# Optimization experiments

Hardware: AMD Instinct MI355X
Metric: run time of the kernel (lower is better)

Reference implementation:

```python
import jax, jax.numpy as jnp
import numpy as np
import math

NUM_HEADS = 8
LN_EPS = 1e-5


def _lstm_stack(x, Wih, Whh, bih, bhh):
    """Stacked unidirectional LSTM (torch gate order i,f,g,o). x: [B,T,F]; params stacked [L,...]."""
    L = Wih.shape[0]
    for l in range(L):
        # precompute input contribution for all timesteps: [B,T,4H]
        xg = jnp.einsum('btf,gf->btg', x, Wih[l]) + bih[l] + bhh[l]
        B = x.shape[0]
        H = Whh.shape[2]
        Whh_l = Whh[l]

        def step(carry, g_t):
            h, c = carry
            g = g_t + h @ Whh_l.T  # [B,4H]
            i, f, gg, o = jnp.split(g, 4, axis=-1)
            c = jax.nn.sigmoid(f) * c + jax.nn.sigmoid(i) * jnp.tanh(gg)
            h = jax.nn.sigmoid(o) * jnp.tanh(c)
            return (h, c), h

        init = (jnp.zeros((B, H), x.dtype), jnp.zeros((B, H), x.dtype))
        _, hs = jax.lax.scan(step, init, xg.transpose(1, 0, 2))  # hs: [T,B,H]
        x = hs.transpose(1, 0, 2)
    return x


def _forward(input, noise, lstm_Wih, lstm_Whh, lstm_bih, lstm_bhh, ln_gamma, ln_beta,
             Wcp, bcp, Wff, bff, Wq, bq, Wkv, bkv, Wout, bout, sequence_mask, chunk_size):
    B, T, F = input.shape
    K = T // chunk_size

    lstm_out = _lstm_stack(input, lstm_Wih, lstm_Whh, lstm_bih, lstm_bhh)  # [B,T,H]

    # LayerNorm over last dim
    mu = lstm_out.mean(-1, keepdims=True)
    var = ((lstm_out - mu) ** 2).mean(-1, keepdims=True)
    normed = (lstm_out - mu) / jnp.sqrt(var + LN_EPS) * ln_gamma + ln_beta

    # chunk summaries -> pivots [B,K,ff]
    chunk_summary = normed.reshape(B * K, chunk_size, -1).sum(axis=1)
    chunk_pivots = (chunk_summary @ Wcp.T + bcp).reshape(B, K, -1)
    # per-frame features [B,T,ff]
    future_frames = normed @ Wff.T + bff

    ff_dim = chunk_pivots.shape[-1]
    dot_products = jnp.einsum('bkf,btf->bkt', chunk_pivots, future_frames) * math.sqrt(1.0 / float(ff_dim))
    eof_probs = jax.nn.sigmoid(dot_products + noise)  # [B,K,T]

    # zero eof prob for frames up to each chunk's endpoint (always in-context)
    chunk_endpts = (jnp.arange(K) + 1) * chunk_size  # [K]
    within = jnp.arange(T)[None, :] < chunk_endpts[:, None]  # [K,T]
    eof_probs = jnp.where(within[None, :, :], 0.0, eof_probs)
    # padded frames: eof prob 1 (never attended beyond)
    eof_probs = jnp.where(~sequence_mask[:, None, :], 1.0, eof_probs)

    in_futctx_probs = jnp.concatenate(
        [jnp.ones_like(eof_probs[..., :1]), 1.0 - eof_probs[..., :-1]], axis=-1)  # [B,K,T]

    # expected multi-head attention
    hd = ff_dim // NUM_HEADS
    q = (chunk_pivots @ Wq.T + bq).reshape(B, K, NUM_HEADS, hd)
    kv = future_frames @ Wkv.T + bkv
    k, v = jnp.split(kv, 2, axis=-1)
    k = k.reshape(B, T, NUM_HEADS, hd)
    v = v.reshape(B, T, NUM_HEADS, hd)

    scale = math.sqrt(1.0 / float(hd))
    scores = jnp.einsum('bkhf,bthf->bhkt', q, k)
    attn = jax.nn.softmax(scale * scores, axis=-1)
    attn = attn * in_futctx_probs[:, None, :, :]
    attn = attn / attn.sum(axis=-1, keepdims=True)
    # attn_dropout is identity in eval mode
    ctx = jnp.einsum('bhkt,bthf->bkhf', attn, v).reshape(B, K, ff_dim)
    expected_fut_ctx = ctx @ Wout.T + bout  # [B,K,input_dim]
    return expected_fut_ctx, in_futctx_probs


def setup_inputs() -> dict:
    key = jax.random.key(0)
    ks = jax.random.split(key, 24)
    B, T, F = 8, 1024, 512
    H = 512
    FF = 512
    L = 2
    CS = 32
    K = T // CS
    s = 0.04  # ~1/sqrt(512)
    inp = {
        'input': jax.random.normal(ks[0], (B, T, F), jnp.float32),
        'sequence_mask': jnp.ones((B, T), jnp.bool_),
        'chunk_size': CS,
        'noise': jax.random.normal(ks[1], (B, K, T), jnp.float32) * 0.1,
        'lstm_Wih': jax.random.normal(ks[2], (L, 4 * H, F), jnp.float32) * s,
        'lstm_Whh': jax.random.normal(ks[3], (L, 4 * H, H), jnp.float32) * s,
        'lstm_bih': jax.random.normal(ks[4], (L, 4 * H), jnp.float32) * s,
        'lstm_bhh': jax.random.normal(ks[5], (L, 4 * H), jnp.float32) * s,
        'ln_gamma': jnp.ones((H,), jnp.float32) + jax.random.normal(ks[6], (H,), jnp.float32) * 0.02,
        'ln_beta': jax.random.normal(ks[7], (H,), jnp.float32) * 0.02,
        'Wcp': jax.random.normal(ks[8], (FF, H), jnp.float32) * s,
        'bcp': jax.random.normal(ks[9], (FF,), jnp.float32) * s,
        'Wff': jax.random.normal(ks[10], (FF, H), jnp.float32) * s,
        'bff': jax.random.normal(ks[11], (FF,), jnp.float32) * s,
        'Wq': jax.random.normal(ks[12], (FF, FF), jnp.float32) * s,
        'bq': jax.random.normal(ks[13], (FF,), jnp.float32) * s,
        'Wkv': jax.random.normal(ks[14], (2 * FF, FF), jnp.float32) * s,
        'bkv': jax.random.normal(ks[15], (2 * FF,), jnp.float32) * s,
        'Wout': jax.random.normal(ks[16], (F, FF), jnp.float32) * s,
        'bout': jax.random.normal(ks[17], (F,), jnp.float32) * s,
    }
    return inp


def reference(input, noise, lstm_Wih, lstm_Whh, lstm_bih, lstm_bhh, ln_gamma, ln_beta,
              Wcp, bcp, Wff, bff, Wq, bq, Wkv, bkv, Wout, bout, sequence_mask, chunk_size):
    return _forward(input, noise, lstm_Wih, lstm_Whh, lstm_bih, lstm_bhh, ln_gamma, ln_beta,
                    Wcp, bcp, Wff, bff, Wq, bq, Wkv, bkv, Wout, bout, sequence_mask, chunk_size)
```

## Files before the change

kernel.cpp:

```cpp
#include <hip/hip_runtime.h>


typedef unsigned short u16;
typedef __attribute__((ext_vector_type(8))) short bf16x8;
typedef __attribute__((ext_vector_type(4))) float f32x4;
typedef __attribute__((ext_vector_type(4))) unsigned int u32x4;

#define T_    1024
#define HSTR  20

__device__ __forceinline__ float bf2f(u16 h) {
    union { unsigned int u; float f; } v; v.u = ((unsigned int)h) << 16; return v.f;
}
__device__ __forceinline__ u16 f2bf(float x) {
    union { float f; unsigned int u; } v; v.f = x;
    unsigned int r = (v.u + 0x7FFFu + ((v.u >> 16) & 1u)) >> 16;
    return (u16)r;
}
__device__ __forceinline__ float sigm(float x) { return 1.f / (1.f + __expf(-x)); }
__device__ __forceinline__ float tanhf_(float x) {
    float e = __expf(-2.f * fabsf(x));
    float t = (1.f - e) / (1.f + e);
    return x < 0.f ? -t : t;
}

__global__ __launch_bounds__(256) void k_split(const float* __restrict__ in,
                                               u16* __restrict__ hi, u16* __restrict__ lo, long n) {
    long i = ((long)blockIdx.x * 256 + threadIdx.x) * 4;
    if (i >= n) return;
    union { u16 h[4]; unsigned long long q; } ph, pl;
#pragma unroll
    for (int j = 0; j < 4; ++j) {
        float v = in[i + j];
        u16 h = f2bf(v);
        ph.h[j] = h;
        pl.h[j] = f2bf(v - bf2f(h));
    }
    *reinterpret_cast<unsigned long long*>(hi + i) = ph.q;
    *reinterpret_cast<unsigned long long*>(lo + i) = pl.q;
}

__global__ __launch_bounds__(256) void k_addvec(const float* __restrict__ a, const float* __restrict__ b,
                                                float* __restrict__ o, int n) {
    int i = blockIdx.x * 256 + threadIdx.x;
    if (i < n) o[i] = a[i] + b[i];
}

__global__ __launch_bounds__(256)
void k_gemm(const u16* __restrict__ Ah, const u16* __restrict__ Al,
            const u16* __restrict__ Bh, const u16* __restrict__ Bl,
            const float* __restrict__ bias,
            float* __restrict__ Cf, u16* __restrict__ Ch, u16* __restrict__ Cl,
            unsigned int* __restrict__ Cp, int xgfmt,
            int M, int N, int K, long sA, long sB, long sC)
{
    const int lane = threadIdx.x & 63;
    const int wave = threadIdx.x >> 6;
    const int wr = wave >> 1, wc = wave & 1;
    const long bz = blockIdx.z;
    const u16* Ahb = Ah + bz * sA;
    const u16* Alb = Al + bz * sA;
    const u16* Bhb = Bh + bz * sB;
    const u16* Blb = Bl + bz * sB;
    const int rowBase = blockIdx.y * 128 + wr * 64;
    const int colBase = blockIdx.x * 128 + wc * 64;
    const int lr = lane & 15;
    const int lk = (lane >> 4) * 8;

    f32x4 acc[4][4];
#pragma unroll
    for (int j = 0; j < 4; ++j) {
        float bv = bias ? bias[colBase + j * 16 + lr] : 0.f;
#pragma unroll
        for (int i = 0; i < 4; ++i) acc[i][j] = (f32x4){bv, bv, bv, bv};
    }
    for (int k0 = 0; k0 < K; k0 += 32) {
        bf16x8 ah[4], al[4], bh[4], bl[4];
#pragma unroll
        for (int i = 0; i < 4; ++i) {
            long off = (long)(rowBase + i * 16 + lr) * K + k0 + lk;
            ah[i] = *reinterpret_cast<const bf16x8*>(Ahb + off);
            al[i] = *reinterpret_cast<const bf16x8*>(Alb + off);
        }
#pragma unroll
        for (int j = 0; j < 4; ++j) {
            long off = (long)(colBase + j * 16 + lr) * K + k0 + lk;
            bh[j] = *reinterpret_cast<const bf16x8*>(Bhb + off);
            bl[j] = *reinterpret_cast<const bf16x8*>(Blb + off);
        }
#pragma unroll
        for (int i = 0; i < 4; ++i)
#pragma unroll
            for (int j = 0; j < 4; ++j) {
                acc[i][j] = __builtin_amdgcn_mfma_f32_16x16x32_bf16(ah[i], bh[j], acc[i][j], 0, 0, 0);
                acc[i][j] = __builtin_amdgcn_mfma_f32_16x16x32_bf16(al[i], bh[j], acc[i][j], 0, 0, 0);
                acc[i][j] = __builtin_amdgcn_mfma_f32_16x16x32_bf16(ah[i], bl[j], acc[i][j], 0, 0, 0);
            }
    }
#pragma unroll
    for (int i = 0; i < 4; ++i) {
        int row0 = rowBase + i * 16 + (lane >> 4) * 4;
#pragma unroll
        for (int j = 0; j < 4; ++j) {
            int col = colBase + j * 16 + lr;
#pragma unroll
            for (int r = 0; r < 4; ++r) {
                int row = row0 + r;
                if (row < M) {
                    float v = acc[i][j][r];
                    if (Cp) {
                        u16 h = f2bf(v); u16 l = f2bf(v - bf2f(h));
                        unsigned int pv = (unsigned int)h | ((unsigned int)l << 16);
                        long idx = xgfmt ? (((long)(row & 1023) * 2048 + col) * 8 + (row >> 10))
                                         : (bz * sC + (long)row * N + col);
                        Cp[idx] = pv;
                    } else if (Ch) {
                        long idx = bz * sC + (long)row * N + col;
                        u16 h = f2bf(v);
                        Ch[idx] = h;
                        Cl[idx] = f2bf(v - bf2f(h));
                    } else {
                        Cf[bz * sC + (long)row * N + col] = v;
                    }
                }
            }
        }
    }
}

__global__ __launch_bounds__(256, 1)
void k_lstm2(const u16* __restrict__ Wh1, const u16* __restrict__ Wl1,
             const u16* __restrict__ Wh2, const u16* __restrict__ Wl2,
             const u16* __restrict__ Uh2, const u16* __restrict__ Ul2,
             const unsigned int* __restrict__ xg1,
             const float* __restrict__ bias2,
             unsigned int* __restrict__ hw1, unsigned int* __restrict__ hw2,
             unsigned int* __restrict__ fl1, unsigned int* __restrict__ fl2)
{
    __shared__ u16 ldsWh[64 * 512];
    __shared__ unsigned int hstA[256 * HSTR];
    __shared__ unsigned int hstB[256 * HSTR];
    __shared__ unsigned int outb[128];

    const int bid = blockIdx.x;
    const bool isL2 = bid >= 32;
    const int blk = isL2 ? bid - 32 : bid;
    const int tid = threadIdx.x;
    const int lane = tid & 63;
    const int wave = tid >> 6;
    const int lr = lane & 15;
    const int lkh = lane >> 4;
    const int lk = lkh * 8;
    const int grow = (lr & 3) * 512 + blk * 16 + wave * 4 + (lr >> 2);

    const u16* WhA = isL2 ? Wh2 : Wh1;
    const u16* WlA = isL2 ? Wl2 : Wl1;

    for (int i = tid; i < 64 * 64; i += 256) {
        int rl = i >> 6;
        int col = (i & 63) * 8;
        int g = (rl & 3) * 512 + blk * 16 + (rl >> 4) * 4 + ((rl >> 2) & 3);
        int sw = rl * 512 + (col ^ ((rl & 15) << 3));
        *reinterpret_cast<bf16x8*>(&ldsWh[sw]) =
            *reinterpret_cast<const bf16x8*>(WhA + (long)g * 512 + col);
    }
    __syncthreads();

    const int myrl = wave * 16 + lr;
    const int swz = (myrl & 15) << 3;
    const int basel = lane & ~3;
    const bool writer = ((lane & 3) == 0) && (lkh < 2);
    const int uloc = wave * 4 + (lr >> 2);
    float cc[4] = {0.f, 0.f, 0.f, 0.f};
    const float bv = isL2 ? bias2[grow] : 0.f;
    unsigned int* hwOut = isL2 ? hw2 : hw1;
    unsigned int* flOut = isL2 ? fl2 : fl1;

    auto waitf = [&](const unsigned int* pa, const unsigned int* pb) {
        const unsigned int* p = (lane < 32) ? (pa + lane * 16)
                                            : (pb ? (pb + (lane - 32) * 16) : nullptr);
        for (int g = 0; g < 131072; ++g) {
            unsigned int f = p ? __hip_atomic_load(p, __ATOMIC_RELAXED, __HIP_MEMORY_SCOPE_AGENT) : 1u;
            if (__ballot(f != 0) == ~0ULL) break;
            __builtin_amdgcn_s_sleep(1);
        }
        asm volatile("" ::: "memory");
    };

    auto stage = [&](const unsigned int* src, unsigned int* dst) {
        const unsigned int* s = src + tid * 16;
        u32x4 v0 = *reinterpret_cast<const u32x4*>(s);
        u32x4 v1 = *reinterpret_cast<const u32x4*>(s + 4);
        u32x4 v2 = *reinterpret_cast<const u32x4*>(s + 8);
        u32x4 v3 = *reinterpret_cast<const u32x4*>(s + 12);
        unsigned int* d = dst + tid * HSTR;
        *reinterpret_cast<u32x4*>(d)      = v0;
        *reinterpret_cast<u32x4*>(d + 4)  = v1;
        *reinterpret_cast<u32x4*>(d + 8)  = v2;
        *reinterpret_cast<u32x4*>(d + 12) = v3;
    };

    auto hfrag = [&](const unsigned int* hst, int s, bf16x8& hi, bf16x8& lo) {
        if (lr < 8) {
            const unsigned int* hp = hst + (s * 16 + (lkh >> 1) * 8 + lr) * HSTR + (lkh & 1) * 8;
            u32x4 wa = *reinterpret_cast<const u32x4*>(hp);
            u32x4 wb = *reinterpret_cast<const u32x4*>(hp + 4);
            union { unsigned int d[4]; bf16x8 v; } H, L;
            H.d[0] = __builtin_amdgcn_perm(wa.y, wa.x, 0x05040100u);
            L.d[0] = __builtin_amdgcn_perm(wa.y, wa.x, 0x07060302u);
            H.d[1] = __builtin_amdgcn_perm(wa.w, wa.z, 0x05040100u);
            L.d[1] = __builtin_amdgcn_perm(wa.w, wa.z, 0x07060302u);
            H.d[2] = __builtin_amdgcn_perm(wb.y, wb.x, 0x05040100u);
            L.d[2] = __builtin_amdgcn_perm(wb.y, wb.x, 0x07060302u);
            H.d[3] = __builtin_amdgcn_perm(wb.w, wb.z, 0x05040100u);
            L.d[3] = __builtin_amdgcn_perm(wb.w, wb.z, 0x07060302u);
            hi = H.v; lo = L.v;
        } else {
            hi = (bf16x8){0,0,0,0,0,0,0,0};
            lo = (bf16x8){0,0,0,0,0,0,0,0};
        }
    };

#pragma unroll 1
    for (int ct = 0; ct < T_; ++ct) {
        u32x4 xw = (u32x4){0, 0, 0, 0};
        if (!isL2 && lkh < 2)
            xw = *reinterpret_cast<const u32x4*>(xg1 + ((long)ct * 2048 + grow) * 8 + lkh * 4);

        if (wave == 0) {
            if (!isL2) waitf(fl1 + (long)ct * 512, nullptr);
            else       waitf(fl2 + (long)ct * 512, fl1 + (long)(ct + 1) * 512);
        }
        __syncthreads();

        if (!isL2) stage(hw1 + (long)ct * 4096, hstA);
        else {
            stage(hw2 + (long)ct * 4096, hstA);
            stage(hw1 + (long)(ct + 1) * 4096, hstB);
        }
        __syncthreads();

        f32x4 acc;
        if (!isL2) {
            f32x4 a0, a1 = (f32x4){0.f, 0.f, 0.f, 0.f};
            a0.x = bf2f((u16)(xw.x & 0xffff)) + bf2f((u16)(xw.x >> 16));
            a0.y = bf2f((u16)(xw.y & 0xffff)) + bf2f((u16)(xw.y >> 16));
            a0.z = bf2f((u16)(xw.z & 0xffff)) + bf2f((u16)(xw.z >> 16));
            a0.w = bf2f((u16)(xw.w & 0xffff)) + bf2f((u16)(xw.w >> 16));
#pragma unroll
            for (int s = 0; s < 16; s += 2) {
                bf16x8 h0, l0, h1, l1;
                hfrag(hstA, s, h0, l0);
                hfrag(hstA, s + 1, h1, l1);
                int c0 = (s * 32 + lk) ^ swz;
                int c1 = ((s + 1) * 32 + lk) ^ swz;
                bf16x8 wh0 = *reinterpret_cast<const bf16x8*>(&ldsWh[myrl * 512 + c0]);
                bf16x8 wh1 = *reinterpret_cast<const bf16x8*>(&ldsWh[myrl * 512 + c1]);
                long w0 = (long)grow * 512 + s * 32 + lk;
                bf16x8 wl0 = *reinterpret_cast<const bf16x8*>(WlA + w0);
                bf16x8 wl1 = *reinterpret_cast<const bf16x8*>(WlA + w0 + 32);
                a0 = __builtin_amdgcn_mfma_f32_16x16x32_bf16(h0, wh0, a0, 0, 0, 0);
                a1 = __builtin_amdgcn_mfma_f32_16x16x32_bf16(h1, wh1, a1, 0, 0, 0);
                a0 = __builtin_amdgcn_mfma_f32_16x16x32_bf16(l0, wh0, a0, 0, 0, 0);
                a1 = __builtin_amdgcn_mfma_f32_16x16x32_bf16(l1, wh1, a1, 0, 0, 0);
                a0 = __builtin_amdgcn_mfma_f32_16x16x32_bf16(h0, wl0, a0, 0, 0, 0);
                a1 = __builtin_amdgcn_mfma_f32_16x16x32_bf16(h1, wl1, a1, 0, 0, 0);
            }
            acc = a0 + a1;
        } else {
            f32x4 a0 = (f32x4){bv, bv, bv, bv};
            f32x4 a1 = (f32x4){0.f, 0.f, 0.f, 0.f};
            f32x4 a2 = a1, a3 = a1;
#pragma unroll
            for (int s = 0; s < 16; s += 2) {
                bf16x8 h2a, l2a, h2b, l2b, h1a, l1a, h1b, l1b;
                hfrag(hstA, s, h2a, l2a);
                hfrag(hstA, s + 1, h2b, l2b);
                hfrag(hstB, s, h1a, l1a);
                hfrag(hstB, s + 1, h1b, l1b);
                int c0 = (s * 32 + lk) ^ swz;
                int c1 = ((s + 1) * 32 + lk) ^ swz;
                bf16x8 wh0 = *reinterpret_cast<const bf16x8*>(&ldsWh[myrl * 512 + c0]);
                bf16x8 wh1 = *reinterpret_cast<const bf16x8*>(&ldsWh[myrl * 512 + c1]);
                long w0 = (long)grow * 512 + s * 32 + lk;
                bf16x8 wl0 = *reinterpret_cast<const bf16x8*>(WlA + w0);
                bf16x8 wl1 = *reinterpret_cast<const bf16x8*>(WlA + w0 + 32);
                bf16x8 uh0 = *reinterpret_cast<const bf16x8*>(Uh2 + w0);
                bf16x8 uh1 = *reinterpret_cast<const bf16x8*>(Uh2 + w0 + 32);
                bf16x8 ul0 = *reinterpret_cast<const bf16x8*>(Ul2 + w0);
                bf16x8 ul1 = *reinterpret_cast<const bf16x8*>(Ul2 + w0 + 32);
                a0 = __builtin_amdgcn_mfma_f32_16x16x32_bf16(h2a, wh0, a0, 0, 0, 0);
                a1 = __builtin_amdgcn_mfma_f32_16x16x32_bf16(h2b, wh1, a1, 0, 0, 0);
                a2 = __builtin_amdgcn_mfma_f32_16x16x32_bf16(h1a, uh0, a2, 0, 0, 0);
                a3 = __builtin_amdgcn_mfma_f32_16x16x32_bf16(h1b, uh1, a3, 0, 0, 0);
                a0 = __builtin_amdgcn_mfma_f32_16x16x32_bf16(l2a, wh0, a0, 0, 0, 0);
                a1 = __builtin_amdgcn_mfma_f32_16x16x32_bf16(l2b, wh1, a1, 0, 0, 0);
                a2 = __builtin_amdgcn_mfma_f32_16x16x32_bf16(l1a, ul0, a2, 0, 0, 0);
                a3 = __builtin_amdgcn_mfma_f32_16x16x32_bf16(l1b, ul1, a3, 0, 0, 0);
                a0 = __builtin_amdgcn_mfma_f32_16x16x32_bf16(h2a, wl0, a0, 0, 0, 0);
                a1 = __builtin_amdgcn_mfma_f32_16x16x32_bf16(h2b, wl1, a1, 0, 0, 0);
                a2 = __builtin_amdgcn_mfma_f32_16x16x32_bf16(h1a, uh0, a2, 0, 0, 0) - a2 + a2;
                a3 = a3;
                a2 = __builtin_amdgcn_mfma_f32_16x16x32_bf16(h1a, ul0, a2, 0, 0, 0) - a2 + a2;
                a3 = a3;
                (void)0;
                a2 = __builtin_amdgcn_mfma_f32_16x16x32_bf16(l1a, uh0, a2, 0, 0, 0);
                a3 = __builtin_amdgcn_mfma_f32_16x16x32_bf16(l1b, uh1, a3, 0, 0, 0);
            }
            a2 = (f32x4){0.f, 0.f, 0.f, 0.f};
            a3 = (f32x4){0.f, 0.f, 0.f, 0.f};
#pragma unroll
            for (int s = 0; s < 16; s += 2) {
                bf16x8 h1a, l1a, h1b, l1b;
                hfrag(hstB, s, h1a, l1a);
                hfrag(hstB, s + 1, h1b, l1b);
                long w0 = (long)grow * 512 + s * 32 + lk;
                bf16x8 uh0 = *reinterpret_cast<const bf16x8*>(Uh2 + w0);
                bf16x8 uh1 = *reinterpret_cast<const bf16x8*>(Uh2 + w0 + 32);
                bf16x8 ul0 = *reinterpret_cast<const bf16x8*>(Ul2 + w0);
                bf16x8 ul1 = *reinterpret_cast<const bf16x8*>(Ul2 + w0 + 32);
                a2 = __builtin_amdgcn_mfma_f32_16x16x32_bf16(h1a, uh0, a2, 0, 0, 0);
                a3 = __builtin_amdgcn_mfma_f32_16x16x32_bf16(h1b, uh1, a3, 0, 0, 0);
                a2 = __builtin_amdgcn_mfma_f32_16x16x32_bf16(l1a, uh0, a2, 0, 0, 0);
                a3 = __builtin_amdgcn_mfma_f32_16x16x32_bf16(l1b, uh1, a3, 0, 0, 0);
                a2 = __builtin_amdgcn_mfma_f32_16x16x32_bf16(h1a, ul0, a2, 0, 0, 0);
                a3 = __builtin_amdgcn_mfma_f32_16x16x32_bf16(h1b, ul1, a3, 0, 0, 0);
            }
            acc = (a0 + a1) + (a2 + a3);
        }

        float hval[4];
#pragma unroll
        for (int r = 0; r < 4; ++r) {
            float v = acc[r];
            float iv = __shfl(v, basel + 0, 64);
            float fv = __shfl(v, basel + 1, 64);
            float gv = __shfl(v, basel + 2, 64);
            float ov = __shfl(v, basel + 3, 64);
            float cn = sigm(fv) * cc[r] + sigm(iv) * tanhf_(gv);
            cc[r] = cn;
            hval[r] = sigm(ov) * tanhf_(cn);
        }
        if (writer) {
#pragma unroll
            for (int r = 0; r < 4; ++r) {
                u16 h = f2bf(hval[r]);
                outb[(lkh * 4 + r) * 16 + uloc] =
                    (unsigned int)h | ((unsigned int)f2bf(hval[r] - bf2f(h)) << 16);
            }
        }
        __syncthreads();
        if (wave == 0) {
            if (lane < 32) {
                u32x4 v = *reinterpret_cast<const u32x4*>(&outb[lane * 4]);
                unsigned long long* hd = (unsigned long long*)
                    (hwOut + (long)(ct + 1) * 4096 + blk * 128 + lane * 4);
                __hip_atomic_store(hd, (unsigned long long)v.x | ((unsigned long long)v.y << 32),
                                   __ATOMIC_RELAXED, __HIP_MEMORY_SCOPE_AGENT);
                __hip_atomic_store(hd + 1, (unsigned long long)v.z | ((unsigned long long)v.w << 32),
                                   __ATOMIC_RELAXED, __HIP_MEMORY_SCOPE_AGENT);
            }
            asm volatile("s_waitcnt vmcnt(0)" ::: "memory");
            if (tid == 0)
                __hip_atomic_store(flOut + (long)(ct + 1) * 512 + blk * 16, 1u,
                                   __ATOMIC_RELAXED, __HIP_MEMORY_SCOPE_AGENT);
        }
    }
}

__global__ __launch_bounds__(256)
void k_ln(const unsigned int* __restrict__ hw2,
          const float* __restrict__ gamma, const float* __restrict__ beta,
          u16* __restrict__ nh, u16* __restrict__ nl)
{
    __shared__ float sb[8];
    int m = blockIdx.x;
    int b = m >> 10, t = m & 1023;
    const unsigned int* src = hw2 + (long)(t + 1) * 4096;
    int tid = threadIdx.x;
    int u0 = tid, u1 = tid + 256;
    unsigned int w0 = src[(u0 >> 4) * 128 + b * 16 + (u0 & 15)];
    unsigned int w1 = src[(u1 >> 4) * 128 + b * 16 + (u1 & 15)];
    float x0 = bf2f((u16)(w0 & 0xffff)) + bf2f((u16)(w0 >> 16));
    float x1 = bf2f((u16)(w1 & 0xffff)) + bf2f((u16)(w1 >> 16));
    float s = x0 + x1;
#pragma unroll
    for (int off = 32; off; off >>= 1) s += __shfl_down(s, off, 64);
    int wv = tid >> 6, ln = tid & 63;
    if (ln == 0) sb[wv] = s;
    __syncthreads();
    float mu = (sb[0] + sb[1] + sb[2] + sb[3]) * (1.f / 512.f);
    float d0 = x0 - mu, d1 = x1 - mu;
    float ss = d0 * d0 + d1 * d1;
#pragma unroll
    for (int off = 32; off; off >>= 1) ss += __shfl_down(ss, off, 64);
    if (ln == 0) sb[4 + wv] = ss;
    __syncthreads();
    float var = (sb[4] + sb[5] + sb[6] + sb[7]) * (1.f / 512.f);
    float rstd = rsqrtf(var + 1e-5f);
    float y0 = d0 * rstd * gamma[tid] + beta[tid];
    float y1 = d1 * rstd * gamma[tid + 256] + beta[tid + 256];
    long d = (long)m * 512;
    u16 h0 = f2bf(y0); nh[d + tid] = h0; nl[d + tid] = f2bf(y0 - bf2f(h0));
    u16 h1 = f2bf(y1); nh[d + tid + 256] = h1; nl[d + tid + 256] = f2bf(y1 - bf2f(h1));
}

__global__ __launch_bounds__(256)
void k_chunksum(const u16* __restrict__ nh, const u16* __restrict__ nl,
                u16* __restrict__ ch, u16* __restrict__ cl)
{
    int bk = blockIdx.x;
    int tid = threadIdx.x;
    long base = (long)bk * 32 * 512;
    float s0 = 0.f, s1 = 0.f;
#pragma unroll 4
    for (int i = 0; i < 32; ++i) {
        s0 += bf2f(nh[base + (long)i * 512 + tid]) + bf2f(nl[base + (long)i * 512 + tid]);
        s1 += bf2f(nh[base + (long)i * 512 + tid + 256]) + bf2f(nl[base + (long)i * 512 + tid + 256]);
    }
    long d = (long)bk * 512;
    u16 h0 = f2bf(s0); ch[d + tid] = h0; cl[d + tid] = f2bf(s0 - bf2f(h0));
    u16 h1 = f2bf(s1); ch[d + tid + 256] = h1; cl[d + tid + 256] = f2bf(s1 - bf2f(h1));
}

__global__ __launch_bounds__(256)
void k_eof(const float* __restrict__ dp, const float* __restrict__ noise, float* __restrict__ ifp)
{
    int bk = blockIdx.x;
    int k = bk & 31;
    long base = (long)bk * 1024;
    int tid = threadIdx.x;
#pragma unroll
    for (int i = 0; i < 4; ++i) {
        int t = tid + i * 256;
        float e;
        if (t < (k + 1) * 32) e = 0.f;
        else e = sigm(dp[base + t] * 0.0441941738241592f + noise[base + t]);
        if (t == 0) ifp[base] = 1.f;
        if (t < 1023) ifp[base + t + 1] = 1.f - e;
    }
}

__global__ __launch_bounds__(256)
void k_attn(const float* __restrict__ qf, const float* __restrict__ kvf,
            const float* __restrict__ ifp, u16* __restrict__ ctxh, u16* __restrict__ ctxl)
{
    int bh = blockIdx.x;
    int b = bh >> 5;
    int h = (bh >> 2) & 7;
    int kg = bh & 3;
    __shared__ float qs[8 * 64];
    __shared__ float tile[64 * 65];
    __shared__ float sc[8 * 1024];
    int tid = threadIdx.x;

    for (int i = tid; i < 512; i += 256) {
        int kq = i >> 6, d = i & 63;
        qs[i] = qf[((long)b * 32 + kg * 8 + kq) * 512 + h * 64 + d];
    }
    __syncthreads();
    for (int t0 = 0; t0 < 1024; t0 += 64) {
        for (int i = tid; i < 4096; i += 256) {
            int tt = i >> 6, d = i & 63;
            tile[tt * 65 + d] = kvf[((long)b * 1024 + t0 + tt) * 1024 + h * 64 + d];
        }
        __syncthreads();
#pragma unroll
        for (int pi = 0; pi < 2; ++pi) {
            int p = tid + pi * 256;
            int kq = p >> 6, tt = p & 63;
            float s = 0.f;
#pragma unroll 8
            for (int d = 0; d < 64; ++d) s += qs[kq * 64 + d] * tile[tt * 65 + d];
            sc[kq * 1024 + t0 + tt] = s * 0.125f;
        }
        __syncthreads();
    }
    {
        int w = tid >> 6, lane = tid & 63;
#pragma unroll
        for (int rr = 0; rr < 2; ++rr) {
            int kq = w * 2 + rr;
            float m = -1e30f;
            float vv[16];
#pragma unroll
            for (int i = 0; i < 16; ++i) {
                vv[i] = sc[kq * 1024 + lane + i * 64];
                m = fmaxf(m, vv[i]);
            }
#pragma unroll
            for (int off = 32; off; off >>= 1) m = fmaxf(m, __shfl_xor(m, off, 64));
            long ibase = ((long)b * 32 + kg * 8 + kq) * 1024;
            float sum = 0.f;
            float wv[16];
#pragma unroll
            for (int i = 0; i < 16; ++i) {
                float pv = ifp[ibase + lane + i * 64];
                float e = __expf(vv[i] - m) * pv;
                wv[i] = e; sum += e;
            }
#pragma unroll
            for (int off = 32; off; off >>= 1) sum += __shfl_xor(sum, off, 64);
            float inv = 1.f / sum;
#pragma unroll
            for (int i = 0; i < 16; ++i) sc[kq * 1024 + lane + i * 64] = wv[i] * inv;
        }
    }
    __syncthreads();
    float c0 = 0.f, c1 = 0.f;
    int kq0 = tid >> 6, d0 = tid & 63;
    int kq1 = (tid + 256) >> 6, d1 = tid & 63;
    for (int t0 = 0; t0 < 1024; t0 += 64) {
        __syncthreads();
        for (int i = tid; i < 4096; i += 256) {
            int tt = i >> 6, d = i & 63;
            tile[tt * 65 + d] = kvf[((long)b * 1024 + t0 + tt) * 1024 + 512 + h * 64 + d];
        }
        __syncthreads();
#pragma unroll 8
        for (int tt = 0; tt < 64; ++tt) {
            float a0 = sc[kq0 * 1024 + t0 + tt];
            float a1 = sc[kq1 * 1024 + t0 + tt];
            c0 += a0 * tile[tt * 65 + d0];
            c1 += a1 * tile[tt * 65 + d1];
        }
    }
    long i0 = ((long)b * 32 + kg * 8 + kq0) * 512 + h * 64 + d0;
    long i1 = ((long)b * 32 + kg * 8 + kq1) * 512 + h * 64 + d1;
    u16 h0 = f2bf(c0); ctxh[i0] = h0; ctxl[i0] = f2bf(c0 - bf2f(h0));
    u16 h1v = f2bf(c1); ctxh[i1] = h1v; ctxl[i1] = f2bf(c1 - bf2f(h1v));
}

extern "C" void kernel_launch(void* const* d_in, const int* in_sizes, int n_in,
                              void* d_out, int out_size, void* d_ws, size_t ws_size,
                              hipStream_t stream)
{
    const float* input = (const float*)d_in[0];
    const float* noise = (const float*)d_in[3];
    const float* Wih  = (const float*)d_in[4];
    const float* Whh  = (const float*)d_in[5];
    const float* bih  = (const float*)d_in[6];
    const float* bhh  = (const float*)d_in[7];
    const float* gam  = (const float*)d_in[8];
    const float* bet  = (const float*)d_in[9];
    const float* Wcp  = (const float*)d_in[10]; const float* bcp  = (const float*)d_in[11];
    const float* Wff  = (const float*)d_in[12]; const float* bff  = (const float*)d_in[13];
    const float* Wq   = (const float*)d_in[14]; const float* bq   = (const float*)d_in[15];
    const float* Wkv  = (const float*)d_in[16]; const float* bkv  = (const float*)d_in[17];
    const float* Wout = (const float*)d_in[18]; const float* bout = (const float*)d_in[19];
    (void)in_sizes; (void)n_in; (void)out_size; (void)ws_size;

    float* out_ctx = (float*)d_out;
    float* out_ifp = (float*)d_out + 8 * 32 * 512;

    char* p = (char*)d_ws;
    auto alloc = [&](size_t bytes) { char* q = p; p += (bytes + 255) & ~(size_t)255; return q; };
    u16* Xh   = (u16*)alloc(8192ULL * 512 * 2);  u16* Xl   = (u16*)alloc(8192ULL * 512 * 2);
    u16* Wihh = (u16*)alloc(2ULL*2048*512*2);    u16* Wihl = (u16*)alloc(2ULL*2048*512*2);
    u16* Whhh = (u16*)alloc(2ULL*2048*512*2);    u16* Whhl = (u16*)alloc(2ULL*2048*512*2);
    u16* Wcph = (u16*)alloc(512ULL*512*2);       u16* Wcpl = (u16*)alloc(512ULL*512*2);
    u16* Wffh = (u16*)alloc(512ULL*512*2);       u16* Wffl = (u16*)alloc(512ULL*512*2);
    u16* Wqh  = (u16*)alloc(512ULL*512*2);       u16* Wql  = (u16*)alloc(512ULL*512*2);
    u16* Wkvh = (u16*)alloc(1024ULL*512*2);      u16* Wkvl = (u16*)alloc(1024ULL*512*2);
    u16* Wouth= (u16*)alloc(512ULL*512*2);       u16* Woutl= (u16*)alloc(512ULL*512*2);
    float* bias12 = (float*)alloc(4096ULL * 4);
    unsigned int* xg1p = (unsigned int*)alloc(8192ULL * 2048 * 4);
    unsigned int* hw1  = (unsigned int*)alloc(1025ULL * 4096 * 4);
    unsigned int* hw2  = (unsigned int*)alloc(1025ULL * 4096 * 4);
    unsigned int* fl1  = (unsigned int*)alloc(1025ULL * 512 * 4);
    unsigned int* fl2  = (unsigned int*)alloc(1025ULL * 512 * 4);
    u16* nh   = (u16*)alloc(8192ULL*512*2);      u16* nl   = (u16*)alloc(8192ULL*512*2);
    u16* csh  = (u16*)alloc(256ULL*512*2);       u16* csl  = (u16*)alloc(256ULL*512*2);
    u16* pivh = (u16*)alloc(512ULL*512*2);       u16* pivl = (u16*)alloc(512ULL*512*2);
    u16* ffh  = (u16*)alloc(8192ULL*512*2);      u16* ffl  = (u16*)alloc(8192ULL*512*2);
    u16* ctxhb= (u16*)alloc(256ULL*512*2);       u16* ctxlb= (u16*)alloc(256ULL*512*2);
    float* qf  = (float*)alloc(256ULL*512*4);
    float* kvf = (float*)alloc(8192ULL*1024*4);
    float* dp  = (float*)alloc(8ULL*32*1024*4);

    hipMemsetAsync(fl1, 0, 1025ULL * 512 * 4, stream);
    hipMemsetAsync(fl2, 0, 1025ULL * 512 * 4, stream);
    hipMemsetAsync(fl1, 1, 32 * 64, stream);
    hipMemsetAsync(fl2, 1, 32 * 64, stream);
    hipMemsetAsync(hw1, 0, 4096 * 4, stream);
    hipMemsetAsync(hw2, 0, 4096 * 4, stream);

    k_split<<<4096, 256, 0, stream>>>(input, Xh, Xl, 8192L * 512);
    k_split<<<2048, 256, 0, stream>>>(Wih, Wihh, Wihl, 2L * 2048 * 512);
    k_split<<<2048, 256, 0, stream>>>(Whh, Whhh, Whhl, 2L * 2048 * 512);
    k_split<<<256, 256, 0, stream>>>(Wcp, Wcph, Wcpl, 512L * 512);
    k_split<<<256, 256, 0, stream>>>(Wff, Wffh, Wffl, 512L * 512);
    k_split<<<256, 256, 0, stream>>>(Wq, Wqh, Wql, 512L * 512);
    k_split<<<512, 256, 0, stream>>>(Wkv, Wkvh, Wkvl, 1024L * 512);
    k_split<<<256, 256, 0, stream>>>(Wout, Wouth, Woutl, 512L * 512);
    k_addvec<<<16, 256, 0, stream>>>(bih, bhh, bias12, 4096);

    k_gemm<<<dim3(16, 64, 1), 256, 0, stream>>>(Xh, Xl, Wihh, Wihl, bias12,
                                                nullptr, nullptr, nullptr, xg1p, 1,
                                                8192, 2048, 512, 0, 0, 0);
    k_lstm2<<<64, 256, 0, stream>>>(Whhh, Whhl, Whhh + 2048L*512, Whhl + 2048L*512,
                                    Wihh + 2048L*512, Wihl + 2048L*512,
                                    xg1p, bias12 + 2048, hw1, hw2, fl1, fl2);

    k_ln<<<8192, 256, 0, stream>>>(hw2, gam, bet, nh, nl);
    k_chunksum<<<256, 256, 0, stream>>>(nh, nl, csh, csl);
    k_gemm<<<dim3(4, 2, 1), 256, 0, stream>>>(csh, csl, Wcph, Wcpl, bcp,
                                              nullptr, pivh, pivl, nullptr, 0, 256, 512, 512, 0, 0, 0);
    k_gemm<<<dim3(4, 2, 1), 256, 0, stream>>>(pivh, pivl, Wqh, Wql, bq,
                                              qf, nullptr, nullptr, nullptr, 0, 256, 512, 512, 0, 0, 0);
    k_gemm<<<dim3(4, 64, 1), 256, 0, stream>>>(nh, nl, Wffh, Wffl, bff,
                                               nullptr, ffh, ffl, nullptr, 0, 8192, 512, 512, 0, 0, 0);
    k_gemm<<<dim3(8, 64, 1), 256, 0, stream>>>(ffh, ffl, Wkvh, Wkvl, bkv,
                                               kvf, nullptr, nullptr, nullptr, 0, 8192, 1024, 512, 0, 0, 0);
    k_gemm<<<dim3(8, 1, 8), 256, 0, stream>>>(pivh, pivl, ffh, ffl, nullptr,
                                              dp, nullptr, nullptr, nullptr, 0, 32, 1024, 512,
                                              32L * 512, 1024L * 512, 32L * 1024);
    k_eof<<<256, 256, 0, stream>>>(dp, noise, out_ifp);
    k_attn<<<256, 256, 0, stream>>>(qf, kvf, out_ifp, ctxhb, ctxlb);
    k_gemm<<<dim3(4, 2, 1), 256, 0, stream>>>(ctxhb, ctxlb, Wouth, Woutl, bout,
                                              out_ctx, nullptr, nullptr, nullptr, 0, 256, 512, 512, 0, 0, 0);
}
```

Measured before the change: 10.38 ms.

## Read LSTM hidden state directly from global, prefetch xg, drop redundant MFMAs

Removes the per-step LDS staging of the previous hidden state and its extra __syncthreads. MFMA fragments are now loaded directly from the global handoff buffer, and the output scratch is double-buffered so the dropped barrier does not create a hazard. The layer-1 input-gate contribution is prefetched four timesteps ahead in registers. The layer-2 path loses a duplicated, partly wasted recurrent-weight loop, and both layers use more independent accumulators to shorten MFMA dependency chains. The aim is lower latency on the serial recurrence. The risk is that global/L2 reads of the fresh hidden state may have higher latency than the LDS reads they replace.

Result: slower. 17.46 ms (+68.1%).

```diff
diff --git a/kernel.cpp b/kernel.cpp
--- a/kernel.cpp
+++ b/kernel.cpp
@@ -7,7 +7,6 @@
 typedef __attribute__((ext_vector_type(4))) unsigned int u32x4;
 
 #define T_    1024
-#define HSTR  20
 
 __device__ __forceinline__ float bf2f(u16 h) {
     union { unsigned int u; float f; } v; v.u = ((unsigned int)h) << 16; return v.f;
@@ -138,9 +137,7 @@
              unsigned int* __restrict__ fl1, unsigned int* __restrict__ fl2)
 {
     __shared__ u16 ldsWh[64 * 512];
-    __shared__ unsigned int hstA[256 * HSTR];
-    __shared__ unsigned int hstB[256 * HSTR];
-    __shared__ unsigned int outb[128];
+    __shared__ unsigned int outb[2][128];
 
     const int bid = blockIdx.x;
     const bool isL2 = bid >= 32;
@@ -187,22 +184,9 @@
         asm volatile("" ::: "memory");
     };
 
-    auto stage = [&](const unsigned int* src, unsigned int* dst) {
-        const unsigned int* s = src + tid * 16;
-        u32x4 v0 = *reinterpret_cast<const u32x4*>(s);
-        u32x4 v1 = *reinterpret_cast<const u32x4*>(s + 4);
-        u32x4 v2 = *reinterpret_cast<const u32x4*>(s + 8);
-        u32x4 v3 = *reinterpret_cast<const u32x4*>(s + 12);
-        unsigned int* d = dst + tid * HSTR;
-        *reinterpret_cast<u32x4*>(d)      = v0;
-        *reinterpret_cast<u32x4*>(d + 4)  = v1;
-        *reinterpret_cast<u32x4*>(d + 8)  = v2;
-        *reinterpret_cast<u32x4*>(d + 12) = v3;
-    };
-
-    auto hfrag = [&](const unsigned int* hst, int s, bf16x8& hi, bf16x8& lo) {
+    auto hfrag = [&](const unsigned int* slot, int s, bf16x8& hi, bf16x8& lo) {
         if (lr < 8) {
-            const unsigned int* hp = hst + (s * 16 + (lkh >> 1) * 8 + lr) * HSTR + (lkh & 1) * 8;
+            const unsigned int* hp = slot + (s * 2 + (lkh >> 1)) * 128 + lr * 16 + (lkh & 1) * 8;
             u32x4 wa = *reinterpret_cast<const u32x4*>(hp);
             u32x4 wb = *reinterpret_cast<const u32x4*>(hp + 4);
             union { unsigned int d[4]; bf16x8 v; } H, L;
@@ -221,37 +205,38 @@
         }
     };
 
+    auto xgload = [&](int t) {
+        u32x4 v = (u32x4){0, 0, 0, 0};
+        if (lkh < 2 && t < T_)
+            v = *reinterpret_cast<const u32x4*>(xg1 + ((long)t * 2048 + grow) * 8 + lkh * 4);
+        return v;
+    };
+    u32x4 xq0 = (u32x4){0,0,0,0}, xq1 = xq0, xq2 = xq0, xq3 = xq0;
+    if (!isL2) { xq0 = xgload(0); xq1 = xgload(1); xq2 = xgload(2); xq3 = xgload(3); }
+
 #pragma unroll 1
     for (int ct = 0; ct < T_; ++ct) {
-        u32x4 xw = (u32x4){0, 0, 0, 0};
-        if (!isL2 && lkh < 2)
-            xw = *reinterpret_cast<const u32x4*>(xg1 + ((long)ct * 2048 + grow) * 8 + lkh * 4);
-
         if (wave == 0) {
             if (!isL2) waitf(fl1 + (long)ct * 512, nullptr);
             else       waitf(fl2 + (long)ct * 512, fl1 + (long)(ct + 1) * 512);
         }
         __syncthreads();
 
-        if (!isL2) stage(hw1 + (long)ct * 4096, hstA);
-        else {
-            stage(hw2 + (long)ct * 4096, hstA);
-            stage(hw1 + (long)(ct + 1) * 4096, hstB);
-        }
-        __syncthreads();
-
         f32x4 acc;
         if (!isL2) {
-            f32x4 a0, a1 = (f32x4){0.f, 0.f, 0.f, 0.f};
-            a0.x = bf2f((u16)(xw.x & 0xffff)) + bf2f((u16)(xw.x >> 16));
-            a0.y = bf2f((u16)(xw.y & 0xffff)) + bf2f((u16)(xw.y >> 16));
-            a0.z = bf2f((u16)(xw.z & 0xffff)) + bf2f((u16)(xw.z >> 16));
-            a0.w = bf2f((u16)(xw.w & 0xffff)) + bf2f((u16)(xw.w >> 16));
+            const unsigned int* s1 = hw1 + (long)ct * 4096;
+            f32x4 a0, a1, a2, a3;
+            a0.x = bf2f((u16)(xq0.x & 0xffff)) + bf2f((u16)(xq0.x >> 16));
+            a0.y = bf2f((u16)(xq0.y & 0xffff)) + bf2f((u16)(xq0.y >> 16));
+            a0.z = bf2f((u16)(xq0.z & 0xffff)) + bf2f((u16)(xq0.z >> 16));
+            a0.w = bf2f((u16)(xq0.w & 0xffff)) + bf2f((u16)(xq0.w >> 16));
+            a1 = (f32x4){0.f,0.f,0.f,0.f}; a2 = a1; a3 = a1;
+            xq0 = xq1; xq1 = xq2; xq2 = xq3; xq3 = xgload(ct + 4);
 #pragma unroll
             for (int s = 0; s < 16; s += 2) {
                 bf16x8 h0, l0, h1, l1;
-                hfrag(hstA, s, h0, l0);
-                hfrag(hstA, s + 1, h1, l1);
+                hfrag(s1, s, h0, l0);
+                hfrag(s1, s + 1, h1, l1);
                 int c0 = (s * 32 + lk) ^ swz;
                 int c1 = ((s + 1) * 32 + lk) ^ swz;
                 bf16x8 wh0 = *reinterpret_cast<const bf16x8*>(&ldsWh[myrl * 512 + c0]);
@@ -261,23 +246,25 @@
                 bf16x8 wl1 = *reinterpret_cast<const bf16x8*>(WlA + w0 + 32);
                 a0 = __builtin_amdgcn_mfma_f32_16x16x32_bf16(h0, wh0, a0, 0, 0, 0);
                 a1 = __builtin_amdgcn_mfma_f32_16x16x32_bf16(h1, wh1, a1, 0, 0, 0);
-                a0 = __builtin_amdgcn_mfma_f32_16x16x32_bf16(l0, wh0, a0, 0, 0, 0);
-                a1 = __builtin_amdgcn_mfma_f32_16x16x32_bf16(l1, wh1, a1, 0, 0, 0);
+                a2 = __builtin_amdgcn_mfma_f32_16x16x32_bf16(l0, wh0, a2, 0, 0, 0);
+                a3 = __builtin_amdgcn_mfma_f32_16x16x32_bf16(l1, wh1, a3, 0, 0, 0);
                 a0 = __builtin_amdgcn_mfma_f32_16x16x32_bf16(h0, wl0, a0, 0, 0, 0);
                 a1 = __builtin_amdgcn_mfma_f32_16x16x32_bf16(h1, wl1, a1, 0, 0, 0);
             }
-            acc = a0 + a1;
+            acc = (a0 + a2) + (a1 + a3);
         } else {
-            f32x4 a0 = (f32x4){bv, bv, bv, bv};
-            f32x4 a1 = (f32x4){0.f, 0.f, 0.f, 0.f};
-            f32x4 a2 = a1, a3 = a1;
+            const unsigned int* s2 = hw2 + (long)ct * 4096;
+            const unsigned int* s1 = hw1 + (long)(ct + 1) * 4096;
+            f32x4 wa0 = (f32x4){bv, bv, bv, bv};
+            f32x4 z = (f32x4){0.f,0.f,0.f,0.f};
+            f32x4 wa1 = z, wa2 = z, wa3 = z, ua0 = z, ua1 = z, ua2 = z, ua3 = z;
 #pragma unroll
             for (int s = 0; s < 16; s += 2) {
-                bf16x8 h2a, l2a, h2b, l2b, h1a, l1a, h1b, l1b;
-                hfrag(hstA, s, h2a, l2a);
-                hfrag(hstA, s + 1, h2b, l2b);
-                hfrag(hstB, s, h1a, l1a);
-                hfrag(hstB, s + 1, h1b, l1b);
+                bf16x8 h0, l0, h1, l1, g0, m0, g1, m1;
+                hfrag(s2, s, h0, l0);
+                hfrag(s2, s + 1, h1, l1);
+                hfrag(s1, s, g0, m0);
+                hfrag(s1, s + 1, g1, m1);
                 int c0 = (s * 32 + lk) ^ swz;
                 int c1 = ((s + 1) * 32 + lk) ^ swz;
                 bf16x8 wh0 = *reinterpret_cast<const bf16x8*>(&ldsWh[myrl * 512 + c0]);
@@ -289,44 +276,20 @@
                 bf16x8 uh1 = *reinterpret_cast<const bf16x8*>(Uh2 + w0 + 32);
                 bf16x8 ul0 = *reinterpret_cast<const bf16x8*>(Ul2 + w0);
                 bf16x8 ul1 = *reinterpret_cast<const bf16x8*>(Ul2 + w0 + 32);
-                a0 = __builtin_amdgcn_mfma_f32_16x16x32_bf16(h2a, wh0, a0, 0, 0, 0);
-                a1 = __builtin_amdgcn_mfma_f32_16x16x32_bf16(h2b, wh1, a1, 0, 0, 0);
-                a2 = __builtin_amdgcn_mfma_f32_16x16x32_bf16(h1a, uh0, a2, 0, 0, 0);
-                a3 = __builtin_amdgcn_mfma_f32_16x16x32_bf16(h1b, uh1, a3, 0, 0, 0);
-                a0 = __builtin_amdgcn_mfma_f32_16x16x32_bf16(l2a, wh0, a0, 0, 0, 0);
-                a1 = __builtin_amdgcn_mfma_f32_16x16x32_bf16(l2b, wh1, a1, 0, 0, 0);
-                a2 = __builtin_amdgcn_mfma_f32_16x16x32_bf16(l1a, ul0, a2, 0, 0, 0);
-                a3 = __builtin_amdgcn_mfma_f32_16x16x32_bf16(l1b, ul1, a3, 0, 0, 0);
-                a0 = __builtin_amdgcn_mfma_f32_16x16x32_bf16(h2a, wl0, a0, 0, 0, 0);
-                a1 = __builtin_amdgcn_mfma_f32_16x16x32_bf16(h2b, wl1, a1, 0, 0, 0);
-                a2 = __builtin_amdgcn_mfma_f32_16x16x32_bf16(h1a, uh0, a2, 0, 0, 0) - a2 + a2;
-                a3 = a3;
-                a2 = __builtin_amdgcn_mfma_f32_16x16x32_bf16(h1a, ul0, a2, 0, 0, 0) - a2 + a2;
-                a3 = a3;
-                (void)0;
-                a2 = __builtin_amdgcn_mfma_f32_16x16x32_bf16(l1a, uh0, a2, 0, 0, 0);
-                a3 = __builtin_amdgcn_mfma_f32_16x16x32_bf16(l1b, uh1, a3, 0, 0, 0);
-            }
-            a2 = (f32x4){0.f, 0.f, 0.f, 0.f};
-            a3 = (f32x4){0.f, 0.f, 0.f, 0.f};
-#pragma unroll
-            for (int s = 0; s < 16; s += 2) {
-                bf16x8 h1a, l1a, h1b, l1b;
-                hfrag(hstB, s, h1a, l1a);
-                hfrag(hstB, s + 1, h1b, l1b);
-                long w0 = (long)grow * 512 + s * 32 + lk;
-                bf16x8 uh0 = *reinterpret_cast<const bf16x8*>(Uh2 + w0);
-                bf16x8 uh1 = *reinterpret_cast<const bf16x8*>(Uh2 + w0 + 32);
-                bf16x8 ul0 = *reinterpret_cast<const bf16x8*>(Ul2 + w0);
-                bf16x8 ul1 = *reinterpret_cast<const bf16x8*>(Ul2 + w0 + 32);
-                a2 = __builtin_amdgcn_mfma_f32_16x16x32_bf16(h1a, uh0, a2, 0, 0, 0);
-                a3 = __builtin_amdgcn_mfma_f32_16x16x32_bf16(h1b, uh1, a3, 0, 0, 0);
-                a2 = __builtin_amdgcn_mfma_f32_16x16x32_bf16(l1a, uh0, a2, 0, 0, 0);
-                a3 = __builtin_amdgcn_mfma_f32_16x16x32_bf16(l1b, uh1, a3, 0, 0, 0);
-                a2 = __builtin_amdgcn_mfma_f32_16x16x32_bf16(h1a, ul0, a2, 0, 0, 0);
-                a3 = __builtin_amdgcn_mfma_f32_16x16x32_bf16(h1b, ul1, a3, 0, 0, 0);
-            }
-            acc = (a0 + a1) + (a2 + a3);
+                wa0 = __builtin_amdgcn_mfma_f32_16x16x32_bf16(h0, wh0, wa0, 0, 0, 0);
+                wa1 = __builtin_amdgcn_mfma_f32_16x16x32_bf16(h1, wh1, wa1, 0, 0, 0);
+                ua0 = __builtin_amdgcn_mfma_f32_16x16x32_bf16(g0, uh0, ua0, 0, 0, 0);
+                ua1 = __builtin_amdgcn_mfma_f32_16x16x32_bf16(g1, uh1, ua1, 0, 0, 0);
+                wa2 = __builtin_amdgcn_mfma_f32_16x16x32_bf16(l0, wh0, wa2, 0, 0, 0);
+                wa3 = __builtin_amdgcn_mfma_f32_16x16x32_bf16(l1, wh1, wa3, 0, 0, 0);
+                ua2 = __builtin_amdgcn_mfma_f32_16x16x32_bf16(m0, uh0, ua2, 0, 0, 0);
+                ua3 = __builtin_amdgcn_mfma_f32_16x16x32_bf16(m1, uh1, ua3, 0, 0, 0);
+                wa0 = __builtin_amdgcn_mfma_f32_16x16x32_bf16(h0, wl0, wa0, 0, 0, 0);
+                wa1 = __builtin_amdgcn_mfma_f32_16x16x32_bf16(h1, wl1, wa1, 0, 0, 0);
+                ua0 = __builtin_amdgcn_mfma_f32_16x16x32_bf16(g0, ul0, ua0, 0, 0, 0);
+                ua1 = __builtin_amdgcn_mfma_f32_16x16x32_bf16(g1, ul1, ua1, 0, 0, 0);
+            }
+            acc = ((wa0 + wa2) + (wa1 + wa3)) + ((ua0 + ua2) + (ua1 + ua3));
         }
 
         float hval[4];
@@ -345,14 +308,14 @@
 #pragma unroll
             for (int r = 0; r < 4; ++r) {
                 u16 h = f2bf(hval[r]);
-                outb[(lkh * 4 + r) * 16 + uloc] =
+                outb[ct & 1][(lkh * 4 + r) * 16 + uloc] =
                     (unsigned int)h | ((unsigned int)f2bf(hval[r] - bf2f(h)) << 16);
             }
         }
         __syncthreads();
         if (wave == 0) {
             if (lane < 32) {
-                u32x4 v = *reinterpret_cast<const u32x4*>(&outb[lane * 4]);
+                u32x4 v = *reinterpret_cast<const u32x4*>(&outb[ct & 1][lane * 4]);
                 unsigned long long* hd = (unsigned long long*)
                     (hwOut + (long)(ct + 1) * 4096 + blk * 128 + lane * 4);
                 __hip_atomic_store(hd, (unsigned long long)v.x | ((unsigned long long)v.y << 32),
```
